# Kernel optimization log

Measured on AMD Instinct MI355X. Metric: run time of the kernel, lower is better.

The kernel has to match this reference:

```python
import jax, jax.numpy as jnp
import numpy as np

N, E, D, H = 100000, 20000, 64, 4
NNZ = 500000
NEG_SLOPE_ATT = 0.2   # PyG HypergraphConv attention leaky_relu slope
NEG_SLOPE_FFN = 0.01  # nn.LeakyReLU default
LN_EPS = 1e-5


def setup_inputs() -> dict:
    key = jax.random.key(0)
    ks = jax.random.split(key, 10)
    s = 0.05
    return {
        "x": jax.random.normal(ks[0], (N, D), jnp.float32),
        "adj_row": jax.random.randint(ks[1], (NNZ,), 0, N),
        "adj_col": jax.random.randint(ks[2], (NNZ,), 0, E),
        "adj_val": jax.random.uniform(ks[3], (NNZ,), jnp.float32) + 0.1,
        "num_edges": E,
        "lin_w": jax.random.normal(ks[4], (H * D, D), jnp.float32) * s,
        "att": jax.random.normal(ks[5], (1, H, 2 * D), jnp.float32) * s,
        "bias": jnp.zeros((D,), jnp.float32),
        "ln1_g": jnp.ones((D,), jnp.float32),
        "ln1_b": jnp.zeros((D,), jnp.float32),
        "ln2_g": jnp.ones((D,), jnp.float32),
        "ln2_b": jnp.zeros((D,), jnp.float32),
        "w1": jax.random.normal(ks[6], (D, D), jnp.float32) * s,
        "b1": jnp.zeros((D,), jnp.float32),
        "w2": jax.random.normal(ks[7], (D, D), jnp.float32) * s,
        "b2": jnp.zeros((D,), jnp.float32),
    }


def _layer_norm(x, g, b):
    mu = jnp.mean(x, axis=-1, keepdims=True)
    var = jnp.mean((x - mu) ** 2, axis=-1, keepdims=True)
    return (x - mu) * jax.lax.rsqrt(var + LN_EPS) * g + b


def _hypergraph_layer(x, adj_row, adj_col, adj_val, num_edges,
                      lin_w, att, bias, ln1_g, ln1_b, ln2_g, ln2_b,
                      w1, b1, w2, b2):
    n = x.shape[0]
    # --- get_hyperedge_representation: omega = diag(1/colsum) @ H^T @ x ---
    colsum = jax.ops.segment_sum(adj_val, adj_col, num_segments=num_edges)  # [E]
    omega = jax.ops.segment_sum(adj_val[:, None] * x[adj_row], adj_col,
                                num_segments=num_edges) / colsum[:, None]  # [E, D]
    # --- HypergraphConv (use_attention=True, concat=False) ---
    xh = (x @ lin_w.T).reshape(n, H, D)              # [N, H, D]
    eh = (omega @ lin_w.T).reshape(num_edges, H, D)  # [E, H, D]
    att_x, att_e = att[0, :, :D], att[0, :, D:]      # [H, D] each
    s_n = jnp.einsum('nhd,hd->nh', xh, att_x)        # [N, H]
    s_e = jnp.einsum('ehd,hd->eh', eh, att_e)        # [E, H]
    alpha = jax.nn.leaky_relu(s_n[adj_row] + s_e[adj_col], NEG_SLOPE_ATT)  # [NNZ, H]
    # softmax over incidences grouped by hyperedge (attention_mode='node')
    amax = jax.ops.segment_max(alpha, adj_col, num_segments=num_edges)
    ea = jnp.exp(alpha - amax[adj_col])
    alpha = ea / jax.ops.segment_sum(ea, adj_col, num_segments=num_edges)[adj_col]
    # degree normalizations D (node) and B (hyperedge)
    d_deg = jax.ops.segment_sum(adj_val[adj_col], adj_row, num_segments=n)
    d_inv = jnp.where(d_deg > 0, 1.0 / d_deg, 0.0)
    b_deg = jax.ops.segment_sum(jnp.ones_like(adj_val), adj_col, num_segments=num_edges)
    b_inv = jnp.where(b_deg > 0, 1.0 / b_deg, 0.0)
    # pass 1: nodes -> hyperedges  (norm_i = B at target edge)
    msg1 = b_inv[adj_col][:, None, None] * xh[adj_row] * alpha[:, :, None]
    edge_out = jax.ops.segment_sum(msg1, adj_col, num_segments=num_edges)  # [E,H,D]
    # pass 2: hyperedges -> nodes  (norm_i = D at target node)
    msg2 = d_inv[adj_row][:, None, None] * edge_out[adj_col] * alpha[:, :, None]
    node_out = jax.ops.segment_sum(msg2, adj_row, num_segments=n)  # [N,H,D]
    conv = jnp.mean(node_out, axis=1) + bias  # concat=False -> head mean
    # --- residual + norm + FFN (Linear, Linear, LeakyReLU) ---
    h = _layer_norm(x + conv, ln1_g, ln1_b)
    ffn = jax.nn.leaky_relu((h @ w1.T + b1) @ w2.T + b2, NEG_SLOPE_FFN)
    return _layer_norm(h + ffn, ln2_g, ln2_b)


def reference(x, adj_row, adj_col, adj_val, num_edges, lin_w, att, bias,
              ln1_g, ln1_b, ln2_g, ln2_b, w1, b1, w2, b2):
    return _hypergraph_layer(x, adj_row, adj_col, adj_val, num_edges,
                             lin_w, att, bias, ln1_g, ln1_b, ln2_g, ln2_b,
                             w1, b1, w2, b2)
```

## Files before the change

kernel.cpp:

```cpp
#include <hip/hip_runtime.h>

#define N_NODES 100000
#define N_EDGES 20000
#define DIM 64
#define HEADS 4
#define NNZ_ 500000
#define LNEPS 1e-5f

__device__ __forceinline__ float wsum64(float v){
#pragma unroll
  for (int off = 32; off; off >>= 1) v += __shfl_xor(v, off);
  return v;
}
__device__ __forceinline__ float wmax64(float v){
#pragma unroll
  for (int off = 32; off; off >>= 1) v = fmaxf(v, __shfl_xor(v, off));
  return v;
}
__device__ __forceinline__ float lrelu2(float a){ return a > 0.f ? a : 0.2f*a; }

__device__ __forceinline__ unsigned bfpack(float a, float b){
  unsigned ua = __float_as_uint(a), ub = __float_as_uint(b);
  ua += 0x7fffu + ((ua >> 16) & 1u);
  ub += 0x7fffu + ((ub >> 16) & 1u);
  return (ua >> 16) | (ub & 0xffff0000u);
}

__global__ __launch_bounds__(256) void k_hist(const int* __restrict__ row,
                                              const int* __restrict__ col,
                                              const float* __restrict__ val,
                                              int* __restrict__ ecnt, int* __restrict__ ncnt,
                                              float* __restrict__ colsum, float* __restrict__ ddeg){
  int i = blockIdx.x*256 + threadIdx.x;
  if (i >= NNZ_) return;
  int c = col[i], r = row[i];
  atomicAdd(&ecnt[c], 1);
  atomicAdd(&ncnt[r], 1);
  atomicAdd(&colsum[c], val[i]);
  atomicAdd(&ddeg[r], val[c]);
}

__device__ __forceinline__ void scanA_body(const int* cnt, int* ptr, int* bsum,
                                           int n, int blk){
  __shared__ int wsums[16];
  int idx = blk*1024 + threadIdx.x;
  int lane = threadIdx.x & 63, wid = threadIdx.x >> 6;
  int v = (idx < n) ? cnt[idx] : 0;
  int s = v;
#pragma unroll
  for (int off = 1; off < 64; off <<= 1){
    int t = __shfl_up(s, off);
    if (lane >= off) s += t;
  }
  if (lane == 63) wsums[wid] = s;
  __syncthreads();
  if (wid == 0 && lane < 16){
    int ws = wsums[lane];
    int t = ws;
#pragma unroll
    for (int off = 1; off < 16; off <<= 1){
      int u = __shfl_up(t, off);
      if (lane >= off) t += u;
    }
    wsums[lane] = t - ws;
  }
  __syncthreads();
  if (idx < n) ptr[idx] = wsums[wid] + s - v;
  if (threadIdx.x == 1023) bsum[blk] = wsums[15] + s;
}

__global__ __launch_bounds__(1024) void k_scanA2(const int* __restrict__ ecnt,
                                                 int* __restrict__ colptr,
                                                 int* __restrict__ bsumE, int nbE,
                                                 const int* __restrict__ ncnt,
                                                 int* __restrict__ rowptr,
                                                 int* __restrict__ bsumN){
  int b = blockIdx.x;
  if (b < nbE) scanA_body(ecnt, colptr, bsumE, N_EDGES, b);
  else         scanA_body(ncnt, rowptr, bsumN, N_NODES, b - nbE);
}

__device__ __forceinline__ void scanB_body(int* bsum, int nb, int* ptr, int n){
  __shared__ int sh[256];
  int t = threadIdx.x;
  int v = (t < nb) ? bsum[t] : 0;
  sh[t] = v;
  __syncthreads();
  for (int off = 1; off < 256; off <<= 1){
    int u = (t >= off) ? sh[t-off] : 0;
    __syncthreads();
    sh[t] += u;
    __syncthreads();
  }
  if (t < nb) bsum[t] = sh[t] - v;
  if (t == nb-1) ptr[n] = sh[t];
}

__global__ __launch_bounds__(256) void k_scanB2(int* __restrict__ bsumE, int nbE,
                                                int* __restrict__ colptr,
                                                int* __restrict__ bsumN, int nbN,
                                                int* __restrict__ rowptr){
  if (blockIdx.x == 0) scanB_body(bsumE, nbE, colptr, N_EDGES);
  else                 scanB_body(bsumN, nbN, rowptr, N_NODES);
}

__global__ __launch_bounds__(1024) void k_scanC2(int* __restrict__ colptr,
                                                 const int* __restrict__ bsumE, int nbE,
                                                 int* __restrict__ rowptr,
                                                 const int* __restrict__ bsumN){
  int b = blockIdx.x;
  if (b < nbE){
    int idx = b*1024 + threadIdx.x;
    if (idx < N_EDGES) colptr[idx] += bsumE[b];
  } else {
    int idx = (b - nbE)*1024 + threadIdx.x;
    if (idx < N_NODES) rowptr[idx] += bsumN[b - nbE];
  }
}

__global__ __launch_bounds__(256) void k_scatter(const int* __restrict__ row,
                                                 const int* __restrict__ col,
                                                 const float* __restrict__ val,
                                                 const int* __restrict__ colptr,
                                                 const int* __restrict__ rowptr,
                                                 int* __restrict__ ecur, int* __restrict__ ncur,
                                                 int* __restrict__ rowC, float* __restrict__ valC,
                                                 int* __restrict__ rposC, int* __restrict__ colR){
  int i = blockIdx.x*256 + threadIdx.x;
  if (i >= NNZ_) return;
  int c = col[i], r = row[i];
  int p = atomicAdd(&ecur[c], 1);
  int q = atomicAdd(&ncur[r], 1);
  int cpos = colptr[c] + p;
  int rpos = rowptr[r] + q;
  rowC[cpos] = r;
  valC[cpos] = val[i];
  rposC[cpos] = rpos;
  colR[rpos] = c;
}

__global__ __launch_bounds__(256) void k_watt(const float* __restrict__ lin_w,
                                              const float* __restrict__ att,
                                              float* __restrict__ wattx,
                                              float* __restrict__ watte){
  int j = threadIdx.x;
  int h = j >> 6;
  float sx = 0.f, se = 0.f;
#pragma unroll
  for (int d = 0; d < DIM; ++d){
    float w = lin_w[(h*DIM + d)*DIM + (j & 63)];
    sx = fmaf(att[h*2*DIM + d],       w, sx);
    se = fmaf(att[h*2*DIM + DIM + d], w, se);
  }
  wattx[j] = sx;
  watte[j] = se;
}

__global__ __launch_bounds__(256) void k_wfold(const float* __restrict__ w1,
                                               const float* __restrict__ w2,
                                               const float* __restrict__ b1,
                                               const float* __restrict__ b2,
                                               float* __restrict__ Wf,
                                               float* __restrict__ bp){
  int tid = threadIdx.x;
#pragma unroll
  for (int m = 0; m < 16; ++m){
    int idx = m*256 + tid;
    int o = idx >> 6, k = idx & 63;
    float s = 0.f;
#pragma unroll
    for (int i = 0; i < 64; ++i)
      s = fmaf(w2[o*64 + i], w1[i*64 + k], s);
    Wf[idx] = s;
  }
  if (tid < 64){
    float s = b2[tid];
#pragma unroll
    for (int i = 0; i < 64; ++i)
      s = fmaf(w2[tid*64 + i], b1[i], s);
    bp[tid] = s;
  }
}

__global__ __launch_bounds__(128) void k_pre(const float* __restrict__ x,
                                             const float* __restrict__ wattx,
                                             const float* __restrict__ watte,
                                             float4* __restrict__ snpe){
  int lane = threadIdx.x & 63, wid = threadIdx.x >> 6;
  int n = blockIdx.x*2 + wid;
  if (n >= N_NODES) return;
  float xv = x[(size_t)n*DIM + lane];
  float s0 = wsum64(xv*wattx[lane]);
  float s1 = wsum64(xv*wattx[64+lane]);
  float s2 = wsum64(xv*wattx[128+lane]);
  float s3 = wsum64(xv*wattx[192+lane]);
  float p0 = wsum64(xv*watte[lane]);
  float p1 = wsum64(xv*watte[64+lane]);
  float p2 = wsum64(xv*watte[128+lane]);
  float p3 = wsum64(xv*watte[192+lane]);
  if (lane == 0){
    snpe[2*(size_t)n    ] = make_float4(s0,s1,s2,s3);
    snpe[2*(size_t)n + 1] = make_float4(p0,p1,p2,p3);
  }
}

__global__ __launch_bounds__(128) void k_softagg(const int* __restrict__ colptr,
                                                 const int* __restrict__ rowC,
                                                 const float* __restrict__ valC,
                                                 const int* __restrict__ rposC,
                                                 const float4* __restrict__ snpe,
                                                 const float* __restrict__ colsum,
                                                 const float* __restrict__ x,
                                                 float4* __restrict__ alphaC,
                                                 float4* __restrict__ alphaR,
                                                 float* __restrict__ agg){
  __shared__ float4 aSh[128];
  int lane = threadIdx.x & 63, wid = threadIdx.x >> 6;
  int e = blockIdx.x*2 + wid;
  if (e >= N_EDGES) return;
  int sb = __builtin_amdgcn_readfirstlane(colptr[e]);
  int cnt = __builtin_amdgcn_readfirstlane(colptr[e+1]) - sb;
  if (cnt == 0) return;
  float rcs = 1.0f / colsum[e];
  float acc0=0,acc1=0,acc2=0,acc3=0;

  if (cnt <= 64){
    bool act = lane < cnt;
    int r = 0, rp = 0; float v = 0.f;
    float4 snv = make_float4(0,0,0,0), p = make_float4(0,0,0,0);
    if (act){
      r = rowC[sb+lane];
      v = valC[sb+lane];
      rp = rposC[sb+lane];
      snv = snpe[2*(size_t)r];
      p   = snpe[2*(size_t)r + 1];
    }
    float se0 = wsum64(v*p.x)*rcs, se1 = wsum64(v*p.y)*rcs,
          se2 = wsum64(v*p.z)*rcs, se3 = wsum64(v*p.w)*rcs;
    float t0 = act ? lrelu2(snv.x+se0) : -1e30f;
    float t1 = act ? lrelu2(snv.y+se1) : -1e30f;
    float t2 = act ? lrelu2(snv.z+se2) : -1e30f;
    float t3 = act ? lrelu2(snv.w+se3) : -1e30f;
    float m0 = wmax64(t0), m1 = wmax64(t1), m2 = wmax64(t2), m3 = wmax64(t3);
    float e0 = act ? __expf(t0-m0) : 0.f;
    float e1 = act ? __expf(t1-m1) : 0.f;
    float e2 = act ? __expf(t2-m2) : 0.f;
    float e3 = act ? __expf(t3-m3) : 0.f;
    float q0 = wsum64(e0), q1 = wsum64(e1), q2 = wsum64(e2), q3 = wsum64(e3);
    float4 a = make_float4(e0/q0, e1/q1, e2/q2, e3/q3);
    if (act) alphaR[rp] = a;
    aSh[wid*64 + lane] = a;

    int k = 0;
    for (; k + 4 <= cnt; k += 4){
      int r0 = rowC[sb+k], r1 = rowC[sb+k+1], r2 = rowC[sb+k+2], r3 = rowC[sb+k+3];
      float4 a0 = aSh[wid*64+k], a1 = aSh[wid*64+k+1],
             a2 = aSh[wid*64+k+2], a3 = aSh[wid*64+k+3];
      float x0 = x[(size_t)r0*DIM + lane];
      float x1 = x[(size_t)r1*DIM + lane];
      float x2 = x[(size_t)r2*DIM + lane];
      float x3 = x[(size_t)r3*DIM + lane];
      acc0 = fmaf(a0.x, x0, acc0); acc1 = fmaf(a0.y, x0, acc1);
      acc2 = fmaf(a0.z, x0, acc2); acc3 = fmaf(a0.w, x0, acc3);
      acc0 = fmaf(a1.x, x1, acc0); acc1 = fmaf(a1.y, x1, acc1);
      acc2 = fmaf(a1.z, x1, acc2); acc3 = fmaf(a1.w, x1, acc3);
      acc0 = fmaf(a2.x, x2, acc0); acc1 = fmaf(a2.y, x2, acc1);
      acc2 = fmaf(a2.z, x2, acc2); acc3 = fmaf(a2.w, x2, acc3);
      acc0 = fmaf(a3.x, x3, acc0); acc1 = fmaf(a3.y, x3, acc1);
      acc2 = fmaf(a3.z, x3, acc2); acc3 = fmaf(a3.w, x3, acc3);
    }
    for (; k < cnt; ++k){
      int r0 = rowC[sb+k];
      float4 a0 = aSh[wid*64+k];
      float x0 = x[(size_t)r0*DIM + lane];
      acc0 = fmaf(a0.x, x0, acc0); acc1 = fmaf(a0.y, x0, acc1);
      acc2 = fmaf(a0.z, x0, acc2); acc3 = fmaf(a0.w, x0, acc3);
    }
  } else {
    int s = sb;
    float a0=0,a1=0,a2=0,a3=0;
    for (int base = 0; base < cnt; base += 64){
      int j = s + base + lane;
      if (base + lane < cnt){
        int r = rowC[j]; float v = valC[j];
        float4 p = snpe[2*(size_t)r + 1];
        a0 = fmaf(v,p.x,a0); a1 = fmaf(v,p.y,a1); a2 = fmaf(v,p.z,a2); a3 = fmaf(v,p.w,a3);
      }
    }
    float se0 = wsum64(a0)*rcs, se1 = wsum64(a1)*rcs, se2 = wsum64(a2)*rcs, se3 = wsum64(a3)*rcs;
    float m0=-1e30f,m1=-1e30f,m2=-1e30f,m3=-1e30f;
    for (int base = 0; base < cnt; base += 64){
      int j = s + base + lane;
      if (base + lane < cnt){
        float4 snv = snpe[2*(size_t)rowC[j]];
        m0 = fmaxf(m0, lrelu2(snv.x+se0)); m1 = fmaxf(m1, lrelu2(snv.y+se1));
        m2 = fmaxf(m2, lrelu2(snv.z+se2)); m3 = fmaxf(m3, lrelu2(snv.w+se3));
      }
    }
    m0 = wmax64(m0); m1 = wmax64(m1); m2 = wmax64(m2); m3 = wmax64(m3);
    float q0=0,q1=0,q2=0,q3=0;
    for (int base = 0; base < cnt; base += 64){
      int j = s + base + lane;
      if (base + lane < cnt){
        float4 snv = snpe[2*(size_t)rowC[j]];
        float e0 = __expf(lrelu2(snv.x+se0)-m0), e1 = __expf(lrelu2(snv.y+se1)-m1);
        float e2 = __expf(lrelu2(snv.z+se2)-m2), e3 = __expf(lrelu2(snv.w+se3)-m3);
        q0+=e0; q1+=e1; q2+=e2; q3+=e3;
        alphaC[j] = make_float4(e0,e1,e2,e3);
      }
    }
    q0 = wsum64(q0); q1 = wsum64(q1); q2 = wsum64(q2); q3 = wsum64(q3);
    float r0 = 1.f/q0, r1 = 1.f/q1, r2 = 1.f/q2, r3 = 1.f/q3;
    for (int base = 0; base < cnt; base += 64){
      int j = s + base + lane;
      if (base + lane < cnt){
        float4 av = alphaC[j];
        av = make_float4(av.x*r0, av.y*r1, av.z*r2, av.w*r3);
        alphaC[j] = av;
        alphaR[rposC[j]] = av;
      }
    }
    for (int k = 0; k < cnt; ++k){
      int rj = rowC[sb+k];
      float4 al = alphaC[sb+k];
      float xv = x[(size_t)rj*DIM + lane];
      acc0 = fmaf(al.x, xv, acc0); acc1 = fmaf(al.y, xv, acc1);
      acc2 = fmaf(al.z, xv, acc2); acc3 = fmaf(al.w, xv, acc3);
    }
  }

  float binv = 1.0f/(float)cnt;
  size_t b = (size_t)e*256;
  agg[b       + lane] = acc0*binv;
  agg[b +  64 + lane] = acc1*binv;
  agg[b + 128 + lane] = acc2*binv;
  agg[b + 192 + lane] = acc3*binv;
}

__global__ __launch_bounds__(256) void k_eoT(const float* __restrict__ agg,
                                             const float* __restrict__ lin_w,
                                             unsigned short* __restrict__ eoTb){
  __shared__ float L[16*260];
  int lane = threadIdx.x & 63, h = threadIdx.x >> 6;
  float w[64];
  const float4* wr = (const float4*)(lin_w + ((size_t)h*64 + lane)*64);
#pragma unroll
  for (int k = 0; k < 16; ++k){
    float4 t = wr[k];
    w[4*k] = t.x; w[4*k+1] = t.y; w[4*k+2] = t.z; w[4*k+3] = t.w;
  }
  int e0 = blockIdx.x*16;
#pragma unroll
  for (int el = 0; el < 16; el += 4){
    float av0 = agg[(size_t)(e0+el  )*256 + h*64 + lane];
    float av1 = agg[(size_t)(e0+el+1)*256 + h*64 + lane];
    float av2 = agg[(size_t)(e0+el+2)*256 + h*64 + lane];
    float av3 = agg[(size_t)(e0+el+3)*256 + h*64 + lane];
    float o0=0.f, o1=0.f, o2=0.f, o3=0.f;
#pragma unroll
    for (int k = 0; k < 64; ++k){
      float wk = w[k];
      o0 = fmaf(__shfl(av0, k), wk, o0);
      o1 = fmaf(__shfl(av1, k), wk, o1);
      o2 = fmaf(__shfl(av2, k), wk, o2);
      o3 = fmaf(__shfl(av3, k), wk, o3);
    }
    L[(el  )*260 + lane*4 + h] = o0;
    L[(el+1)*260 + lane*4 + h] = o1;
    L[(el+2)*260 + lane*4 + h] = o2;
    L[(el+3)*260 + lane*4 + h] = o3;
  }
  __syncthreads();
  int tid = threadIdx.x;
#pragma unroll
  for (int p = 0; p < 4; ++p){
    int el = p*4 + (tid >> 6);
    int l = tid & 63;
    const float* Lr = &L[el*260 + l*4];
    uint2 v;
    v.x = bfpack(Lr[0], Lr[1]);
    v.y = bfpack(Lr[2], Lr[3]);
    *(uint2*)(eoTb + (size_t)(e0+el)*256 + l*4) = v;
  }
}

#define ACC4(J, V, A) { \
  float u0 = __uint_as_float((V).x << 16); \
  float u1 = __uint_as_float((V).x & 0xffff0000u); \
  float u2 = __uint_as_float((V).y << 16); \
  float u3 = __uint_as_float((V).y & 0xffff0000u); \
  acc[J][0] = fmaf(u0, (A).x, acc[J][0]); \
  acc[J][1] = fmaf(u1, (A).y, acc[J][1]); \
  acc[J][2] = fmaf(u2, (A).z, acc[J][2]); \
  acc[J][3] = fmaf(u3, (A).w, acc[J][3]); }

#define SEG(J, KB, KE) do { \
    int k = (KB); \
    for (; k + 4 <= (KE); k += 4){ \
      int c0 = colR[k], c1 = colR[k+1], c2 = colR[k+2], c3 = colR[k+3]; \
      float4 a0 = alphaR[k], a1 = alphaR[k+1], a2 = alphaR[k+2], a3 = alphaR[k+3]; \
      uint2 v0 = *(const uint2*)(eoTb + (size_t)c0*256 + lane*4); \
      uint2 v1 = *(const uint2*)(eoTb + (size_t)c1*256 + lane*4); \
      uint2 v2 = *(const uint2*)(eoTb + (size_t)c2*256 + lane*4); \
      uint2 v3 = *(const uint2*)(eoTb + (size_t)c3*256 + lane*4); \
      ACC4(J, v0, a0); ACC4(J, v1, a1); ACC4(J, v2, a2); ACC4(J, v3, a3); \
    } \
    for (; k < (KE); ++k){ \
      int c0 = colR[k]; float4 a0 = alphaR[k]; \
      uint2 v0 = *(const uint2*)(eoTb + (size_t)c0*256 + lane*4); \
      ACC4(J, v0, a0); \
    } \
  } while(0)

__global__ __launch_bounds__(128) void k_final2(const float* __restrict__ x,
                                                const int* __restrict__ rowptr,
                                                const int* __restrict__ colR,
                                                const float4* __restrict__ alphaR,
                                                const unsigned short* __restrict__ eoTb,
                                                const float* __restrict__ ddeg,
                                                const float* __restrict__ bias,
                                                const float* __restrict__ g1,
                                                const float* __restrict__ b1g,
                                                const float* __restrict__ g2,
                                                const float* __restrict__ b2g,
                                                const float* __restrict__ Wf,
                                                const float* __restrict__ bp,
                                                float* __restrict__ out){
  int lane = threadIdx.x & 63, wid = threadIdx.x >> 6;
  int nbase = blockIdx.x*8 + wid*4;
  int q0 = __builtin_amdgcn_readfirstlane(rowptr[nbase]);
  int q1 = __builtin_amdgcn_readfirstlane(rowptr[nbase+1]);
  int q2 = __builtin_amdgcn_readfirstlane(rowptr[nbase+2]);
  int q3 = __builtin_amdgcn_readfirstlane(rowptr[nbase+3]);
  int q4 = __builtin_amdgcn_readfirstlane(rowptr[nbase+4]);

  float xv[4];
#pragma unroll
  for (int j = 0; j < 4; ++j) xv[j] = x[(size_t)(nbase+j)*DIM + lane];
  float dd0 = ddeg[nbase], dd1 = ddeg[nbase+1], dd2 = ddeg[nbase+2], dd3 = ddeg[nbase+3];

  float acc[4][4];
#pragma unroll
  for (int j = 0; j < 4; ++j)
#pragma unroll
    for (int h = 0; h < 4; ++h) acc[j][h] = 0.f;

  SEG(0, q0, q1);
  SEG(1, q1, q2);
  SEG(2, q2, q3);
  SEG(3, q3, q4);

  float w[64];
  const float4* wr = (const float4*)(Wf + (size_t)lane*64);
#pragma unroll
  for (int k = 0; k < 16; ++k){
    float4 t = wr[k];
    w[4*k] = t.x; w[4*k+1] = t.y; w[4*k+2] = t.z; w[4*k+3] = t.w;
  }
  float biasv = bias[lane], bpv = bp[lane];
  float g1v = g1[lane], b1gv = b1g[lane], g2v = g2[lane], b2gv = b2g[lane];

  float ddv[4] = {dd0, dd1, dd2, dd3};
  float hs[4];
#pragma unroll
  for (int j = 0; j < 4; ++j){
    float dd = ddv[j];
    float dinv = dd > 0.f ? 0.25f/dd : 0.f;
    float conv = (acc[j][0]+acc[j][1]+acc[j][2]+acc[j][3])*dinv;
    float t = xv[j] + conv + biasv;
    float mu = wsum64(t) * (1.f/64.f);
    float dv = t - mu;
    float var = wsum64(dv*dv) * (1.f/64.f);
    hs[j] = dv * rsqrtf(var + LNEPS) * g1v + b1gv;
  }

  float a0 = bpv, a1 = bpv, a2 = bpv, a3 = bpv;
#pragma unroll
  for (int k = 0; k < 64; ++k){
    a0 = fmaf(__shfl(hs[0], k), w[k], a0);
    a1 = fmaf(__shfl(hs[1], k), w[k], a1);
    a2 = fmaf(__shfl(hs[2], k), w[k], a2);
    a3 = fmaf(__shfl(hs[3], k), w[k], a3);
  }

  float fa[4] = {a0, a1, a2, a3};
#pragma unroll
  for (int j = 0; j < 4; ++j){
    int n = nbase + j;
    float ffn = fa[j] > 0.f ? fa[j] : 0.01f*fa[j];
    float t2 = hs[j] + ffn;
    float mu2 = wsum64(t2) * (1.f/64.f);
    float dv2 = t2 - mu2;
    float var2 = wsum64(dv2*dv2) * (1.f/64.f);
    out[(size_t)n*DIM + lane] = dv2 * rsqrtf(var2 + LNEPS) * g2v + b2gv;
  }
}

extern "C" void kernel_launch(void* const* d_in, const int* in_sizes, int n_in,
                              void* d_out, int out_size, void* d_ws, size_t ws_size,
                              hipStream_t stream){
  const float* x     = (const float*)d_in[0];
  const int*   row   = (const int*)d_in[1];
  const int*   col   = (const int*)d_in[2];
  const float* val   = (const float*)d_in[3];
  const float* lin_w = (const float*)d_in[5];
  const float* att   = (const float*)d_in[6];
  const float* bias  = (const float*)d_in[7];
  const float* g1    = (const float*)d_in[8];
  const float* b1g   = (const float*)d_in[9];
  const float* g2    = (const float*)d_in[10];
  const float* b2g   = (const float*)d_in[11];
  const float* w1    = (const float*)d_in[12];
  const float* b1    = (const float*)d_in[13];
  const float* w2    = (const float*)d_in[14];
  const float* b2    = (const float*)d_in[15];
  float* out = (float*)d_out;
  float* ws  = (float*)d_ws;

  constexpr size_t E = N_EDGES, Nn = N_NODES;
  constexpr size_t o_ecnt   = 0;
  constexpr size_t o_ncnt   = o_ecnt + E;
  constexpr size_t o_ecur   = o_ncnt + Nn;
  constexpr size_t o_ncur   = o_ecur + E;
  constexpr size_t o_colsum = o_ncur + Nn;
  constexpr size_t o_ddeg   = o_colsum + E;
  constexpr size_t ZEND     = o_ddeg + Nn;
  constexpr size_t o_colptr = ZEND;
  constexpr size_t o_rowptr = o_colptr + E + 4;
  constexpr size_t o_bsumE  = o_rowptr + Nn + 4;
  constexpr size_t o_bsumN  = o_bsumE + 256;
  constexpr size_t o_rowC   = o_bsumN + 256;
  constexpr size_t o_valC   = o_rowC + NNZ_;
  constexpr size_t o_rposC  = o_valC + NNZ_;
  constexpr size_t o_colR   = o_rposC + NNZ_;
  constexpr size_t o_wattx  = o_colR + NNZ_;
  constexpr size_t o_watte  = o_wattx + 256;
  constexpr size_t o_Wf     = o_watte + 256;
  constexpr size_t o_bp     = o_Wf + 4096;
  constexpr size_t o_snpe   = o_bp + 64;
  constexpr size_t o_alphaC = o_snpe + 8*Nn;
  constexpr size_t o_alphaR = o_alphaC + 4*(size_t)NNZ_;
  constexpr size_t o_agg    = o_alphaR + 4*(size_t)NNZ_;
  constexpr size_t o_eo     = o_agg + 256*E;

  int*    ecnt   = (int*)(ws + o_ecnt);
  int*    ncnt   = (int*)(ws + o_ncnt);
  int*    ecur   = (int*)(ws + o_ecur);
  int*    ncur   = (int*)(ws + o_ncur);
  float*  colsum = ws + o_colsum;
  float*  ddeg   = ws + o_ddeg;
  int*    colptr = (int*)(ws + o_colptr);
  int*    rowptr = (int*)(ws + o_rowptr);
  int*    bsumE  = (int*)(ws + o_bsumE);
  int*    bsumN  = (int*)(ws + o_bsumN);
  int*    rowC   = (int*)(ws + o_rowC);
  float*  valC   = ws + o_valC;
  int*    rposC  = (int*)(ws + o_rposC);
  int*    colR   = (int*)(ws + o_colR);
  float*  wattx  = ws + o_wattx;
  float*  watte  = ws + o_watte;
  float*  Wf     = ws + o_Wf;
  float*  bp     = ws + o_bp;
  float4* snpe   = (float4*)(ws + o_snpe);
  float4* alphaC = (float4*)(ws + o_alphaC);
  float4* alphaR = (float4*)(ws + o_alphaR);
  float*  agg    = ws + o_agg;
  unsigned short* eoTb = (unsigned short*)(ws + o_eo);

  hipMemsetAsync(ws, 0, ZEND*sizeof(float), stream);

  k_hist<<<(NNZ_+255)/256, 256, 0, stream>>>(row, col, val, ecnt, ncnt, colsum, ddeg);

  int nbE = (int)((E + 1023)/1024);
  int nbN = (int)((Nn + 1023)/1024);
  k_scanA2<<<nbE + nbN, 1024, 0, stream>>>(ecnt, colptr, bsumE, nbE, ncnt, rowptr, bsumN);
  k_scanB2<<<2, 256, 0, stream>>>(bsumE, nbE, colptr, bsumN, nbN, rowptr);
  k_scanC2<<<nbE + nbN, 1024, 0, stream>>>(colptr, bsumE, nbE, rowptr, bsumN);

  k_scatter<<<(NNZ_+255)/256, 256, 0, stream>>>(row, col, val, colptr, rowptr,
                                                ecur, ncur, rowC, valC, rposC, colR);

  k_watt<<<1, 256, 0, stream>>>(lin_w, att, wattx, watte);
  k_wfold<<<1, 256, 0, stream>>>(w1, w2, b1, b2, Wf, bp);
  k_pre<<<(int)((Nn+1)/2), 128, 0, stream>>>(x, wattx, watte, snpe);
  k_softagg<<<(int)((E+1)/2), 128, 0, stream>>>(colptr, rowC, valC, rposC, snpe, colsum,
                                                x, alphaC, alphaR, agg);
  k_eoT<<<(int)(E/16), 256, 0, stream>>>(agg, lin_w, eoTb);
  k_final2<<<(int)(Nn/8), 128, 0, stream>>>(x, rowptr, colR, alphaR, eoTb, ddeg,
                                            bias, g1, b1g, g2, b2g, Wf, bp, out);
}
```

Measured before the change: 456.5 us.

## Pack CSR/CSC metadata into int4 records and store gathered operands in bf16

```diff
diff --git a/kernel.cpp b/kernel.cpp
--- a/kernel.cpp
+++ b/kernel.cpp
@@ -24,6 +24,14 @@
   ua += 0x7fffu + ((ua >> 16) & 1u);
   ub += 0x7fffu + ((ub >> 16) & 1u);
   return (ua >> 16) | (ub & 0xffff0000u);
+}
+__device__ __forceinline__ unsigned short bf16of(float f){
+  unsigned u = __float_as_uint(f);
+  u += 0x7fffu + ((u >> 16) & 1u);
+  return (unsigned short)(u >> 16);
+}
+__device__ __forceinline__ float bfup(unsigned short s){
+  return __uint_as_float(((unsigned)s) << 16);
 }
 
 __global__ __launch_bounds__(256) void k_hist(const int* __restrict__ row,
@@ -124,19 +132,13 @@
                                                  const int* __restrict__ colptr,
                                                  const int* __restrict__ rowptr,
                                                  int* __restrict__ ecur, int* __restrict__ ncur,
-                                                 int* __restrict__ rowC, float* __restrict__ valC,
-                                                 int* __restrict__ rposC, int* __restrict__ colR){
+                                                 int4* __restrict__ rvp){
   int i = blockIdx.x*256 + threadIdx.x;
   if (i >= NNZ_) return;
   int c = col[i], r = row[i];
   int p = atomicAdd(&ecur[c], 1);
   int q = atomicAdd(&ncur[r], 1);
-  int cpos = colptr[c] + p;
-  int rpos = rowptr[r] + q;
-  rowC[cpos] = r;
-  valC[cpos] = val[i];
-  rposC[cpos] = rpos;
-  colR[rpos] = c;
+  rvp[colptr[c] + p] = make_int4(r, __float_as_int(val[i]), rowptr[r] + q, 0);
 }
 
 __global__ __launch_bounds__(256) void k_watt(const float* __restrict__ lin_w,
@@ -185,11 +187,13 @@
 __global__ __launch_bounds__(128) void k_pre(const float* __restrict__ x,
                                              const float* __restrict__ wattx,
                                              const float* __restrict__ watte,
-                                             float4* __restrict__ snpe){
+                                             float4* __restrict__ snpe,
+                                             unsigned short* __restrict__ xb){
   int lane = threadIdx.x & 63, wid = threadIdx.x >> 6;
   int n = blockIdx.x*2 + wid;
   if (n >= N_NODES) return;
   float xv = x[(size_t)n*DIM + lane];
+  xb[(size_t)n*DIM + lane] = bf16of(xv);
   float s0 = wsum64(xv*wattx[lane]);
   float s1 = wsum64(xv*wattx[64+lane]);
   float s2 = wsum64(xv*wattx[128+lane]);
@@ -205,15 +209,13 @@
 }
 
 __global__ __launch_bounds__(128) void k_softagg(const int* __restrict__ colptr,
-                                                 const int* __restrict__ rowC,
-                                                 const float* __restrict__ valC,
-                                                 const int* __restrict__ rposC,
+                                                 const int4* __restrict__ rvp,
                                                  const float4* __restrict__ snpe,
                                                  const float* __restrict__ colsum,
-                                                 const float* __restrict__ x,
+                                                 const unsigned short* __restrict__ xb,
                                                  float4* __restrict__ alphaC,
-                                                 float4* __restrict__ alphaR,
-                                                 float* __restrict__ agg){
+                                                 int4* __restrict__ cealpha,
+                                                 unsigned short* __restrict__ aggB){
   __shared__ float4 aSh[128];
   int lane = threadIdx.x & 63, wid = threadIdx.x >> 6;
   int e = blockIdx.x*2 + wid;
@@ -229,9 +231,8 @@
     int r = 0, rp = 0; float v = 0.f;
     float4 snv = make_float4(0,0,0,0), p = make_float4(0,0,0,0);
     if (act){
-      r = rowC[sb+lane];
-      v = valC[sb+lane];
-      rp = rposC[sb+lane];
+      int4 m = rvp[sb+lane];
+      r = m.x; v = __int_as_float(m.y); rp = m.z;
       snv = snpe[2*(size_t)r];
       p   = snpe[2*(size_t)r + 1];
     }
@@ -248,18 +249,19 @@
     float e3 = act ? __expf(t3-m3) : 0.f;
     float q0 = wsum64(e0), q1 = wsum64(e1), q2 = wsum64(e2), q3 = wsum64(e3);
     float4 a = make_float4(e0/q0, e1/q1, e2/q2, e3/q3);
-    if (act) alphaR[rp] = a;
+    if (act)
+      cealpha[rp] = make_int4(e, (int)bfpack(a.x,a.y), (int)bfpack(a.z,a.w), 0);
     aSh[wid*64 + lane] = a;
 
     int k = 0;
     for (; k + 4 <= cnt; k += 4){
-      int r0 = rowC[sb+k], r1 = rowC[sb+k+1], r2 = rowC[sb+k+2], r3 = rowC[sb+k+3];
+      int r0 = rvp[sb+k].x, r1 = rvp[sb+k+1].x, r2 = rvp[sb+k+2].x, r3 = rvp[sb+k+3].x;
       float4 a0 = aSh[wid*64+k], a1 = aSh[wid*64+k+1],
              a2 = aSh[wid*64+k+2], a3 = aSh[wid*64+k+3];
-      float x0 = x[(size_t)r0*DIM + lane];
-      float x1 = x[(size_t)r1*DIM + lane];
-      float x2 = x[(size_t)r2*DIM + lane];
-      float x3 = x[(size_t)r3*DIM + lane];
+      float x0 = bfup(xb[(size_t)r0*DIM + lane]);
+      float x1 = bfup(xb[(size_t)r1*DIM + lane]);
+      float x2 = bfup(xb[(size_t)r2*DIM + lane]);
+      float x3 = bfup(xb[(size_t)r3*DIM + lane]);
       acc0 = fmaf(a0.x, x0, acc0); acc1 = fmaf(a0.y, x0, acc1);
       acc2 = fmaf(a0.z, x0, acc2); acc3 = fmaf(a0.w, x0, acc3);
       acc0 = fmaf(a1.x, x1, acc0); acc1 = fmaf(a1.y, x1, acc1);
@@ -270,9 +272,9 @@
       acc2 = fmaf(a3.z, x3, acc2); acc3 = fmaf(a3.w, x3, acc3);
     }
     for (; k < cnt; ++k){
-      int r0 = rowC[sb+k];
+      int r0 = rvp[sb+k].x;
       float4 a0 = aSh[wid*64+k];
-      float x0 = x[(size_t)r0*DIM + lane];
+      float x0 = bfup(xb[(size_t)r0*DIM + lane]);
       acc0 = fmaf(a0.x, x0, acc0); acc1 = fmaf(a0.y, x0, acc1);
       acc2 = fmaf(a0.z, x0, acc2); acc3 = fmaf(a0.w, x0, acc3);
     }
@@ -282,8 +284,9 @@
     for (int base = 0; base < cnt; base += 64){
       int j = s + base + lane;
       if (base + lane < cnt){
-        int r = rowC[j]; float v = valC[j];
-        float4 p = snpe[2*(size_t)r + 1];
+        int4 m = rvp[j];
+        float v = __int_as_float(m.y);
+        float4 p = snpe[2*(size_t)m.x + 1];
         a0 = fmaf(v,p.x,a0); a1 = fmaf(v,p.y,a1); a2 = fmaf(v,p.z,a2); a3 = fmaf(v,p.w,a3);
       }
     }
@@ -292,7 +295,7 @@
     for (int base = 0; base < cnt; base += 64){
       int j = s + base + lane;
       if (base + lane < cnt){
-        float4 snv = snpe[2*(size_t)rowC[j]];
+        float4 snv = snpe[2*(size_t)rvp[j].x];
         m0 = fmaxf(m0, lrelu2(snv.x+se0)); m1 = fmaxf(m1, lrelu2(snv.y+se1));
         m2 = fmaxf(m2, lrelu2(snv.z+se2)); m3 = fmaxf(m3, lrelu2(snv.w+se3));
       }
@@ -302,7 +305,7 @@
     for (int base = 0; base < cnt; base += 64){
       int j = s + base + lane;
       if (base + lane < cnt){
-        float4 snv = snpe[2*(size_t)rowC[j]];
+        float4 snv = snpe[2*(size_t)rvp[j].x];
         float e0 = __expf(lrelu2(snv.x+se0)-m0), e1 = __expf(lrelu2(snv.y+se1)-m1);
         float e2 = __expf(lrelu2(snv.z+se2)-m2), e3 = __expf(lrelu2(snv.w+se3)-m3);
         q0+=e0; q1+=e1; q2+=e2; q3+=e3;
@@ -317,13 +320,13 @@
         float4 av = alphaC[j];
         av = make_float4(av.x*r0, av.y*r1, av.z*r2, av.w*r3);
         alphaC[j] = av;
-        alphaR[rposC[j]] = av;
+        cealpha[rvp[j].z] = make_int4(e, (int)bfpack(av.x,av.y), (int)bfpack(av.z,av.w), 0);
       }
     }
     for (int k = 0; k < cnt; ++k){
-      int rj = rowC[sb+k];
+      int rj = rvp[sb+k].x;
       float4 al = alphaC[sb+k];
-      float xv = x[(size_t)rj*DIM + lane];
+      float xv = bfup(xb[(size_t)rj*DIM + lane]);
       acc0 = fmaf(al.x, xv, acc0); acc1 = fmaf(al.y, xv, acc1);
       acc2 = fmaf(al.z, xv, acc2); acc3 = fmaf(al.w, xv, acc3);
     }
@@ -331,13 +334,13 @@
 
   float binv = 1.0f/(float)cnt;
   size_t b = (size_t)e*256;
-  agg[b       + lane] = acc0*binv;
-  agg[b +  64 + lane] = acc1*binv;
-  agg[b + 128 + lane] = acc2*binv;
-  agg[b + 192 + lane] = acc3*binv;
-}
-
-__global__ __launch_bounds__(256) void k_eoT(const float* __restrict__ agg,
+  aggB[b       + lane] = bf16of(acc0*binv);
+  aggB[b +  64 + lane] = bf16of(acc1*binv);
+  aggB[b + 128 + lane] = bf16of(acc2*binv);
+  aggB[b + 192 + lane] = bf16of(acc3*binv);
+}
+
+__global__ __launch_bounds__(256) void k_eoT(const unsigned short* __restrict__ aggB,
                                              const float* __restrict__ lin_w,
                                              unsigned short* __restrict__ eoTb){
   __shared__ float L[16*260];
@@ -352,10 +355,10 @@
   int e0 = blockIdx.x*16;
 #pragma unroll
   for (int el = 0; el < 16; el += 4){
-    float av0 = agg[(size_t)(e0+el  )*256 + h*64 + lane];
-    float av1 = agg[(size_t)(e0+el+1)*256 + h*64 + lane];
-    float av2 = agg[(size_t)(e0+el+2)*256 + h*64 + lane];
-    float av3 = agg[(size_t)(e0+el+3)*256 + h*64 + lane];
+    float av0 = bfup(aggB[(size_t)(e0+el  )*256 + h*64 + lane]);
+    float av1 = bfup(aggB[(size_t)(e0+el+1)*256 + h*64 + lane]);
+    float av2 = bfup(aggB[(size_t)(e0+el+2)*256 + h*64 + lane]);
+    float av3 = bfup(aggB[(size_t)(e0+el+3)*256 + h*64 + lane]);
     float o0=0.f, o1=0.f, o2=0.f, o3=0.f;
 #pragma unroll
     for (int k = 0; k < 64; ++k){
@@ -384,38 +387,40 @@
   }
 }
 
-#define ACC4(J, V, A) { \
+#define ACC4(J, V, M) { \
   float u0 = __uint_as_float((V).x << 16); \
   float u1 = __uint_as_float((V).x & 0xffff0000u); \
   float u2 = __uint_as_float((V).y << 16); \
   float u3 = __uint_as_float((V).y & 0xffff0000u); \
-  acc[J][0] = fmaf(u0, (A).x, acc[J][0]); \
-  acc[J][1] = fmaf(u1, (A).y, acc[J][1]); \
-  acc[J][2] = fmaf(u2, (A).z, acc[J][2]); \
-  acc[J][3] = fmaf(u3, (A).w, acc[J][3]); }
+  float ax = __uint_as_float(((unsigned)(M).y) << 16); \
+  float ay = __uint_as_float(((unsigned)(M).y) & 0xffff0000u); \
+  float az = __uint_as_float(((unsigned)(M).z) << 16); \
+  float aw = __uint_as_float(((unsigned)(M).z) & 0xffff0000u); \
+  acc[J][0] = fmaf(u0, ax, acc[J][0]); \
+  acc[J][1] = fmaf(u1, ay, acc[J][1]); \
+  acc[J][2] = fmaf(u2, az, acc[J][2]); \
+  acc[J][3] = fmaf(u3, aw, acc[J][3]); }
 
 #define SEG(J, KB, KE) do { \
     int k = (KB); \
     for (; k + 4 <= (KE); k += 4){ \
-      int c0 = colR[k], c1 = colR[k+1], c2 = colR[k+2], c3 = colR[k+3]; \
-      float4 a0 = alphaR[k], a1 = alphaR[k+1], a2 = alphaR[k+2], a3 = alphaR[k+3]; \
-      uint2 v0 = *(const uint2*)(eoTb + (size_t)c0*256 + lane*4); \
-      uint2 v1 = *(const uint2*)(eoTb + (size_t)c1*256 + lane*4); \
-      uint2 v2 = *(const uint2*)(eoTb + (size_t)c2*256 + lane*4); \
-      uint2 v3 = *(const uint2*)(eoTb + (size_t)c3*256 + lane*4); \
-      ACC4(J, v0, a0); ACC4(J, v1, a1); ACC4(J, v2, a2); ACC4(J, v3, a3); \
+      int4 m0 = cealpha[k], m1 = cealpha[k+1], m2 = cealpha[k+2], m3 = cealpha[k+3]; \
+      uint2 v0 = *(const uint2*)(eoTb + (size_t)m0.x*256 + lane*4); \
+      uint2 v1 = *(const uint2*)(eoTb + (size_t)m1.x*256 + lane*4); \
+      uint2 v2 = *(const uint2*)(eoTb + (size_t)m2.x*256 + lane*4); \
+      uint2 v3 = *(const uint2*)(eoTb + (size_t)m3.x*256 + lane*4); \
+      ACC4(J, v0, m0); ACC4(J, v1, m1); ACC4(J, v2, m2); ACC4(J, v3, m3); \
     } \
     for (; k < (KE); ++k){ \
-      int c0 = colR[k]; float4 a0 = alphaR[k]; \
-      uint2 v0 = *(const uint2*)(eoTb + (size_t)c0*256 + lane*4); \
-      ACC4(J, v0, a0); \
+      int4 m0 = cealpha[k]; \
+      uint2 v0 = *(const uint2*)(eoTb + (size_t)m0.x*256 + lane*4); \
+      ACC4(J, v0, m0); \
     } \
   } while(0)
 
 __global__ __launch_bounds__(128) void k_final2(const float* __restrict__ x,
                                                 const int* __restrict__ rowptr,
-                                                const int* __restrict__ colR,
-                                                const float4* __restrict__ alphaR,
+                                                const int4* __restrict__ cealpha,
                                                 const unsigned short* __restrict__ eoTb,
                                                 const float* __restrict__ ddeg,
                                                 const float* __restrict__ bias,
@@ -529,19 +534,17 @@
   constexpr size_t o_rowptr = o_colptr + E + 4;
   constexpr size_t o_bsumE  = o_rowptr + Nn + 4;
   constexpr size_t o_bsumN  = o_bsumE + 256;
-  constexpr size_t o_rowC   = o_bsumN + 256;
-  constexpr size_t o_valC   = o_rowC + NNZ_;
-  constexpr size_t o_rposC  = o_valC + NNZ_;
-  constexpr size_t o_colR   = o_rposC + NNZ_;
-  constexpr size_t o_wattx  = o_colR + NNZ_;
+  constexpr size_t o_rvp    = (o_bsumN + 256 + 3) & ~(size_t)3;
+  constexpr size_t o_wattx  = o_rvp + 4*(size_t)NNZ_;
   constexpr size_t o_watte  = o_wattx + 256;
   constexpr size_t o_Wf     = o_watte + 256;
   constexpr size_t o_bp     = o_Wf + 4096;
   constexpr size_t o_snpe   = o_bp + 64;
   constexpr size_t o_alphaC = o_snpe + 8*Nn;
-  constexpr size_t o_alphaR = o_alphaC + 4*(size_t)NNZ_;
-  constexpr size_t o_agg    = o_alphaR + 4*(size_t)NNZ_;
-  constexpr size_t o_eo     = o_agg + 256*E;
+  constexpr size_t o_ceal   = o_alphaC + 4*(size_t)NNZ_;
+  constexpr size_t o_xb     = o_ceal + 4*(size_t)NNZ_;
+  constexpr size_t o_aggB   = o_xb + 32*Nn;
+  constexpr size_t o_eo     = o_aggB + 128*E;
 
   int*    ecnt   = (int*)(ws + o_ecnt);
   int*    ncnt   = (int*)(ws + o_ncnt);
@@ -553,18 +556,16 @@
   int*    rowptr = (int*)(ws + o_rowptr);
   int*    bsumE  = (int*)(ws + o_bsumE);
   int*    bsumN  = (int*)(ws + o_bsumN);
-  int*    rowC   = (int*)(ws + o_rowC);
-  float*  valC   = ws + o_valC;
-  int*    rposC  = (int*)(ws + o_rposC);
-  int*    colR   = (int*)(ws + o_colR);
+  int4*   rvp    = (int4*)(ws + o_rvp);
   float*  wattx  = ws + o_wattx;
   float*  watte  = ws + o_watte;
   float*  Wf     = ws + o_Wf;
   float*  bp     = ws + o_bp;
   float4* snpe   = (float4*)(ws + o_snpe);
   float4* alphaC = (float4*)(ws + o_alphaC);
-  float4* alphaR = (float4*)(ws + o_alphaR);
-  float*  agg    = ws + o_agg;
+  int4*   cealpha= (int4*)(ws + o_ceal);
+  unsigned short* xb   = (unsigned short*)(ws + o_xb);
+  unsigned short* aggB = (unsigned short*)(ws + o_aggB);
   unsigned short* eoTb = (unsigned short*)(ws + o_eo);
 
   hipMemsetAsync(ws, 0, ZEND*sizeof(float), stream);
@@ -578,14 +579,14 @@
   k_scanC2<<<nbE + nbN, 1024, 0, stream>>>(colptr, bsumE, nbE, rowptr, bsumN);
 
   k_scatter<<<(NNZ_+255)/256, 256, 0, stream>>>(row, col, val, colptr, rowptr,
-                                                ecur, ncur, rowC, valC, rposC, colR);
+                                                ecur, ncur, rvp);
 
   k_watt<<<1, 256, 0, stream>>>(lin_w, att, wattx, watte);
   k_wfold<<<1, 256, 0, stream>>>(w1, w2, b1, b2, Wf, bp);
-  k_pre<<<(int)((Nn+1)/2), 128, 0, stream>>>(x, wattx, watte, snpe);
-  k_softagg<<<(int)((E+1)/2), 128, 0, stream>>>(colptr, rowC, valC, rposC, snpe, colsum,
-                                                x, alphaC, alphaR, agg);
-  k_eoT<<<(int)(E/16), 256, 0, stream>>>(agg, lin_w, eoTb);
-  k_final2<<<(int)(Nn/8), 128, 0, stream>>>(x, rowptr, colR, alphaR, eoTb, ddeg,
+  k_pre<<<(int)((Nn+1)/2), 128, 0, stream>>>(x, wattx, watte, snpe, xb);
+  k_softagg<<<(int)((E+1)/2), 128, 0, stream>>>(colptr, rvp, snpe, colsum, xb,
+                                                alphaC, cealpha, aggB);
+  k_eoT<<<(int)(E/16), 256, 0, stream>>>(aggB, lin_w, eoTb);
+  k_final2<<<(int)(Nn/8), 128, 0, stream>>>(x, rowptr, cealpha, eoTb, ddeg,
                                             bias, g1, b1g, g2, b2g, Wf, bp, out);
 }
```

Result: no change. 449.6 us (-1.5%).
